# Kernel tuning notes

Measured on AMD Instinct MI355X. Metric: run time of the kernel, lower is better.

## Reference

```python
import jax, jax.numpy as jnp
import numpy as np

D_MODEL = 1024
N_HEADS = 16
D_HEAD = D_MODEL // N_HEADS
D_FF = 4096
B, T = 2, 2048


def layer_norm(x, gamma, beta, eps=1e-5):
    mu = jnp.mean(x, axis=-1, keepdims=True)
    var = jnp.var(x, axis=-1, keepdims=True)
    return (x - mu) * jax.lax.rsqrt(var + eps) * gamma + beta


def setup_inputs() -> dict:
    key = jax.random.key(0)
    ks = jax.random.split(key, 8)
    s = D_MODEL ** -0.5
    return {
        "x": jax.random.normal(ks[0], (B, T, D_MODEL), dtype=jnp.float32),
        "w_qkv": jax.random.normal(ks[1], (D_MODEL, 3 * D_MODEL), dtype=jnp.float32) * s,
        "w_out": jax.random.normal(ks[2], (D_MODEL, D_MODEL), dtype=jnp.float32) * s,
        "ln1_g": jnp.ones((D_MODEL,), jnp.float32),
        "ln1_b": jnp.zeros((D_MODEL,), jnp.float32),
        "ln2_g": jnp.ones((D_MODEL,), jnp.float32),
        "ln2_b": jnp.zeros((D_MODEL,), jnp.float32),
        "w1": jax.random.normal(ks[3], (D_MODEL, D_FF), dtype=jnp.float32) * s,
        "b1": jnp.zeros((D_FF,), jnp.float32),
        "w2": jax.random.normal(ks[4], (D_FF, D_MODEL), dtype=jnp.float32) * (D_FF ** -0.5),
        "b2": jnp.zeros((D_MODEL,), jnp.float32),
    }


def reference(x, w_qkv, w_out, ln1_g, ln1_b, ln2_g, ln2_b, w1, b1, w2, b2):
    Bb, Tt, C = x.shape
    h = layer_norm(x, ln1_g, ln1_b)
    qkv = h @ w_qkv  # [B,T,3C]
    q, k, v = jnp.split(qkv, 3, axis=-1)

    def heads(t):  # [B,T,C] -> [B,H,T,Dh]
        return t.reshape(Bb, Tt, N_HEADS, D_HEAD).transpose(0, 2, 1, 3)

    q, k, v = heads(q), heads(k), heads(v)
    scale = D_HEAD ** -0.5
    attn = jnp.einsum("bhqd,bhkd->bhqk", q, k) * scale
    causal = jnp.tril(jnp.ones((Tt, Tt), dtype=bool))
    attn = jnp.where(causal[None, None], attn, -jnp.inf)
    attn = jax.nn.softmax(attn, axis=-1)
    out = jnp.einsum("bhqk,bhkd->bhqd", attn, v)
    out = out.transpose(0, 2, 1, 3).reshape(Bb, Tt, C)
    x = x + out @ w_out
    h2 = layer_norm(x, ln2_g, ln2_b)
    ff = jax.nn.gelu(h2 @ w1 + b1, approximate=False) @ w2 + b2
    return x + ff
```

## Files before the change

kernel.cpp:

```cpp
#include <hip/hip_runtime.h>
#include <hip/hip_bf16.h>
#include <cstdint>

#define DM 1024
#define DFF 4096
#define NB 2
#define TT 2048
#define NH 16
#define DH 64

typedef unsigned short u16;
typedef __bf16 bf16x8 __attribute__((ext_vector_type(8)));
typedef float f32x4 __attribute__((ext_vector_type(4)));

__device__ __forceinline__ u16 f2b(float f) {
    union { float f; unsigned u; } v; v.f = f;
    unsigned u = v.u;
    return (u16)((u + 0x7FFFu + ((u >> 16) & 1u)) >> 16);
}

__device__ __forceinline__ float b2f(u16 u) {
    union { unsigned x; float f; } v;
    v.x = ((unsigned)u) << 16;
    return v.f;
}

__device__ __forceinline__ unsigned cvtpk(float a, float b) {
    unsigned r;
    asm("v_cvt_pk_bf16_f32 %0, %1, %2" : "=v"(r) : "v"(a), "v"(b));
    return r;
}

__device__ __forceinline__ float gelu_fast(float z) {
    const float u = z * z;
    const float w = z * __builtin_fmaf(u, 0.10294324f, 2.3022082f);
    const float e = exp2f(w);
    const float r = __builtin_amdgcn_rcpf(1.0f + e);
    return z - z * r;
}

__device__ __forceinline__ f32x4 mfma_bf16(bf16x8 a, bf16x8 b, f32x4 c) {
    return __builtin_amdgcn_mfma_f32_16x16x32_bf16(a, b, c, 0, 0, 0);
}

__device__ __forceinline__ void gload_lds16(const void* g, void* l) {
    __builtin_amdgcn_global_load_lds((const __attribute__((address_space(1))) unsigned int*)g,
                                     (__attribute__((address_space(3))) unsigned int*)l, 16, 0, 0);
}

__global__ __launch_bounds__(256) void prep_kernel(
    const float* __restrict__ wqkv, const float* __restrict__ wout,
    const float* __restrict__ w1, const float* __restrict__ w2,
    u16* __restrict__ wqkv_t, u16* __restrict__ wout_t,
    u16* __restrict__ w1_t, u16* __restrict__ w2_t,
    const float* __restrict__ x, const float* __restrict__ g,
    const float* __restrict__ bt, u16* __restrict__ H) {
    __shared__ float t[32][33];
    __shared__ float sb[8];
    const int id = blockIdx.x;
    const int tid = threadIdx.x;
    if (id < 12288) {
        const float* W;
        u16* Wt;
        int K, N, bx, by;
        if (id < 3072) {
            W = wqkv; Wt = wqkv_t; K = 1024; N = 3072; bx = id % 96; by = id / 96;
        } else if (id < 4096) {
            const int t2 = id - 3072;
            W = wout; Wt = wout_t; K = 1024; N = 1024; bx = t2 % 32; by = t2 / 32;
        } else if (id < 8192) {
            const int t2 = id - 4096;
            W = w1; Wt = w1_t; K = 1024; N = 4096; bx = t2 % 128; by = t2 / 128;
        } else {
            const int t2 = id - 8192;
            W = w2; Wt = w2_t; K = 4096; N = 1024; bx = t2 % 32; by = t2 / 32;
        }
        const int tx = tid & 31, ty = tid >> 5;
        const int k0 = by * 32, n0 = bx * 32;
#pragma unroll
        for (int j = 0; j < 4; ++j)
            t[ty + 8 * j][tx] = W[(size_t)(k0 + ty + 8 * j) * N + n0 + tx];
        __syncthreads();
#pragma unroll
        for (int j = 0; j < 4; ++j)
            Wt[(size_t)(n0 + ty + 8 * j) * K + k0 + tx] = f2b(t[tx][ty + 8 * j]);
    } else {
        const int row = id - 12288;
        float4 v = ((const float4*)(x + (size_t)row * DM))[tid];
        float s = v.x + v.y + v.z + v.w;
        float ss = v.x * v.x + v.y * v.y + v.z * v.z + v.w * v.w;
#pragma unroll
        for (int off = 32; off >= 1; off >>= 1) {
            s += __shfl_xor(s, off);
            ss += __shfl_xor(ss, off);
        }
        int w = tid >> 6, lane = tid & 63;
        if (lane == 0) { sb[w] = s; sb[4 + w] = ss; }
        __syncthreads();
        s = sb[0] + sb[1] + sb[2] + sb[3];
        ss = sb[4] + sb[5] + sb[6] + sb[7];
        float mu = s * (1.0f / DM);
        float var = ss * (1.0f / DM) - mu * mu;
        float rstd = rsqrtf(var + 1e-5f);
        float4 gv = ((const float4*)g)[tid];
        float4 bv = ((const float4*)bt)[tid];
        uint2 hv;
        hv.x = cvtpk((v.x - mu) * rstd * gv.x + bv.x, (v.y - mu) * rstd * gv.y + bv.y);
        hv.y = cvtpk((v.z - mu) * rstd * gv.z + bv.z, (v.w - mu) * rstd * gv.w + bv.w);
        ((uint2*)(H + (size_t)row * DM))[tid] = hv;
    }
}

__global__ __launch_bounds__(256) void ln_kernel(const float* __restrict__ X,
                                                 const float* __restrict__ g,
                                                 const float* __restrict__ bt,
                                                 u16* __restrict__ H) {
    int row = blockIdx.x, tid = threadIdx.x;
    float4 v = ((const float4*)(X + (size_t)row * DM))[tid];
    float s = v.x + v.y + v.z + v.w;
    float ss = v.x * v.x + v.y * v.y + v.z * v.z + v.w * v.w;
#pragma unroll
    for (int off = 32; off >= 1; off >>= 1) {
        s += __shfl_xor(s, off);
        ss += __shfl_xor(ss, off);
    }
    __shared__ float sb[8];
    int w = tid >> 6, lane = tid & 63;
    if (lane == 0) { sb[w] = s; sb[4 + w] = ss; }
    __syncthreads();
    s = sb[0] + sb[1] + sb[2] + sb[3];
    ss = sb[4] + sb[5] + sb[6] + sb[7];
    float mu = s * (1.0f / DM);
    float var = ss * (1.0f / DM) - mu * mu;
    float rstd = rsqrtf(var + 1e-5f);
    float4 gv = ((const float4*)g)[tid];
    float4 bv = ((const float4*)bt)[tid];
    uint2 hv;
    hv.x = cvtpk((v.x - mu) * rstd * gv.x + bv.x, (v.y - mu) * rstd * gv.y + bv.y);
    hv.y = cvtpk((v.z - mu) * rstd * gv.z + bv.z, (v.w - mu) * rstd * gv.w + bv.w);
    ((uint2*)(H + (size_t)row * DM))[tid] = hv;
}

__global__ __launch_bounds__(256) void add4_kernel(float* __restrict__ out,
                                                   const float* __restrict__ x1,
                                                   const float* __restrict__ b2,
                                                   const u16* __restrict__ p0,
                                                   const u16* __restrict__ p1,
                                                   const u16* __restrict__ p2,
                                                   const u16* __restrict__ p3, int n4) {
    int idx = blockIdx.x * 256 + threadIdx.x;
    const int stride = gridDim.x * 256;
    for (; idx < n4; idx += stride) {
        float4 a = ((const float4*)x1)[idx];
        const float4 bb = ((const float4*)b2)[idx & 255];
        ushort4 c0 = ((const ushort4*)p0)[idx];
        ushort4 c1 = ((const ushort4*)p1)[idx];
        ushort4 c2 = ((const ushort4*)p2)[idx];
        ushort4 c3 = ((const ushort4*)p3)[idx];
        a.x += bb.x + b2f(c0.x) + b2f(c1.x) + b2f(c2.x) + b2f(c3.x);
        a.y += bb.y + b2f(c0.y) + b2f(c1.y) + b2f(c2.y) + b2f(c3.y);
        a.z += bb.z + b2f(c0.z) + b2f(c1.z) + b2f(c2.z) + b2f(c3.z);
        a.w += bb.w + b2f(c0.w) + b2f(c1.w) + b2f(c2.w) + b2f(c3.w);
        ((float4*)out)[idx] = a;
    }
}

template <int MODE, int SPLIT>
__global__ __launch_bounds__(512, 2) void gemm256(
    const u16* __restrict__ A, const u16* __restrict__ Bt, int M, int N, int K,
    u16* __restrict__ oq, u16* __restrict__ ok, u16* __restrict__ vt,
    const float* __restrict__ bias, u16* __restrict__ outbf,
    u16* __restrict__ pb0, u16* __restrict__ pb1,
    u16* __restrict__ pb2, u16* __restrict__ pb3) {
    __shared__ __align__(16) u16 Alds[2][256][64];
    __shared__ __align__(16) u16 Blds[2][256][64];
    const int tid = threadIdx.x;
    const int lane = tid & 63, w = tid >> 6;
    const int wm = w >> 2, wn = w & 3;
    const int l15 = lane & 15, lg = lane >> 4;
    int bid = blockIdx.x + gridDim.x * blockIdx.y;
    const int nwg = gridDim.x * gridDim.y;
    bid = (bid & 7) * (nwg >> 3) + (bid >> 3);
    int mrow = bid / gridDim.x;
    int ks = 0;
    if constexpr (SPLIT > 1) {
        const int mtiles = (nwg / gridDim.x) / SPLIT;
        ks = mrow / mtiles;
        mrow -= ks * mtiles;
    }
    const int bm = mrow * 256, bn = (bid % gridDim.x) * 256;
    const int kbeg = SPLIT > 1 ? ks * (K / SPLIT) : 0;
    const int srow = tid >> 3, pch = tid & 7;
    const int lc = pch ^ (srow & 7);

    const u16* Ap = A + (size_t)(bm + srow) * K + kbeg + lc * 8;
    const u16* Bp = Bt + (size_t)(bn + srow) * K + kbeg + lc * 8;

    f32x4 acc[8][4] = {};
    bf16x8 bf[4][2];
    const int NT = (K / SPLIT) >> 6;

#define SA256(buf, t)                                                           \
    {                                                                           \
        _Pragma("unroll") for (int j = 0; j < 4; ++j)                           \
            gload_lds16(Ap + (size_t)(64 * j) * K + (t) * 64,                   \
                        &Alds[buf][srow + 64 * j][pch * 8]);                    \
    }
#define SB256(buf, t)                                                           \
    {                                                                           \
        _Pragma("unroll") for (int j = 0; j < 4; ++j)                           \
            gload_lds16(Bp + (size_t)(64 * j) * K + (t) * 64,                   \
                        &Blds[buf][srow + 64 * j][pch * 8]);                    \
    }

#define PHASE(BUF, P, STAGE, WAIT)                                              \
    {                                                                           \
        bf16x8 af[2][2];                                                        \
        _Pragma("unroll") for (int i = 0; i < 2; ++i) {                         \
            const int row = wm * 128 + (2 * (P) + i) * 16 + l15;                \
            _Pragma("unroll") for (int ks_ = 0; ks_ < 2; ++ks_)                 \
                af[i][ks_] =                                                    \
                    *(const bf16x8*)&Alds[BUF][row][((ks_ * 4 + lg) ^ (row & 7)) * 8]; \
        }                                                                       \
        if constexpr ((P) == 0) {                                               \
            _Pragma("unroll") for (int nf = 0; nf < 4; ++nf) {                  \
                const int row = wn * 64 + nf * 16 + l15;                        \
                _Pragma("unroll") for (int ks_ = 0; ks_ < 2; ++ks_)             \
                    bf[nf][ks_] =                                               \
                        *(const bf16x8*)&Blds[BUF][row][((ks_ * 4 + lg) ^ (row & 7)) * 8]; \
            }                                                                   \
        }                                                                       \
        STAGE;                                                                  \
        WAIT;                                                                   \
        __builtin_amdgcn_s_barrier();                                           \
        asm volatile("s_waitcnt lgkmcnt(0)" ::: "memory");                      \
        __builtin_amdgcn_sched_barrier(0);                                      \
        __builtin_amdgcn_s_setprio(1);                                          \
        _Pragma("unroll") for (int i = 0; i < 2; ++i)                           \
            _Pragma("unroll") for (int nf = 0; nf < 4; ++nf)                    \
                _Pragma("unroll") for (int ks_ = 0; ks_ < 2; ++ks_)             \
                    acc[2 * (P) + i][nf] =                                      \
                        mfma_bf16(af[i][ks_], bf[nf][ks_], acc[2 * (P) + i][nf]); \
        __builtin_amdgcn_s_setprio(0);                                          \
        __builtin_amdgcn_s_barrier();                                           \
    }

    SB256(0, 0);
    SA256(0, 0);
    SB256(1, 1);
    asm volatile("s_waitcnt vmcnt(4)" ::: "memory");
    __builtin_amdgcn_sched_barrier(0);
    __builtin_amdgcn_s_barrier();

    for (int it = 0; it < (NT >> 1); ++it) {
        const int t0 = 2 * it;
        const bool more = (t0 + 2 < NT);
        PHASE(0, 0, { SA256(1, t0 + 1); }, {});
        PHASE(0, 1, { if (more) SB256(0, t0 + 2); }, {});
        PHASE(0, 2, {}, {});
        PHASE(0, 3, {}, {
            if (more) { asm volatile("s_waitcnt vmcnt(4)" ::: "memory"); }
            else { asm volatile("s_waitcnt vmcnt(0)" ::: "memory"); }
            __builtin_amdgcn_sched_barrier(0);
        });
        PHASE(1, 0, { if (more) SA256(0, t0 + 2); }, {});
        PHASE(1, 1, { if (more) SB256(1, t0 + 3); }, {});
        PHASE(1, 2, {}, {});
        PHASE(1, 3, {}, {
            if (more) {
                asm volatile("s_waitcnt vmcnt(4)" ::: "memory");
                __builtin_amdgcn_sched_barrier(0);
            }
        });
    }
#undef PHASE
#undef SA256
#undef SB256

    const int m0 = bm + wm * 128, n0 = bn + wn * 64;
#pragma unroll
    for (int mi = 0; mi < 8; ++mi) {
#pragma unroll
        for (int ni = 0; ni < 4; ++ni) {
            if constexpr (MODE == 0) {
                const int n = n0 + ni * 16 + l15;
                const int which = n >> 10;
                const int hh = (n >> 6) & 15, d = n & 63;
                const int mbase = m0 + mi * 16 + 4 * lg;
                const int bb = mbase >> 11, t = mbase & 2047;
                if (which == 2) {
                    uint2 pv;
                    pv.x = cvtpk(acc[mi][ni][0], acc[mi][ni][1]);
                    pv.y = cvtpk(acc[mi][ni][2], acc[mi][ni][3]);
                    *(uint2*)(vt + (((size_t)(bb * NH + hh)) * DH + d) * TT + t) = pv;
                } else {
                    u16* dst = which == 0 ? oq : ok;
                    const float sc = which == 0 ? 0.18033688f : 1.0f;
                    const unsigned p01 = cvtpk(acc[mi][ni][0] * sc, acc[mi][ni][1] * sc);
                    const unsigned p23 = cvtpk(acc[mi][ni][2] * sc, acc[mi][ni][3] * sc);
                    u16* db = dst + (((size_t)(bb * NH + hh)) * TT + t) * DH + d;
                    db[0] = (u16)p01;
                    db[DH] = (u16)(p01 >> 16);
                    db[2 * DH] = (u16)p23;
                    db[3 * DH] = (u16)(p23 >> 16);
                }
            } else if constexpr (MODE == 2) {
                const int n = n0 + ni * 16 + l15;
                const float bn_ = bias[n];
                const float g0 = gelu_fast(acc[mi][ni][0] + bn_);
                const float g1 = gelu_fast(acc[mi][ni][1] + bn_);
                const float g2 = gelu_fast(acc[mi][ni][2] + bn_);
                const float g3 = gelu_fast(acc[mi][ni][3] + bn_);
                const unsigned p01 = cvtpk(g0, g1);
                const unsigned p23 = cvtpk(g2, g3);
                u16* db = outbf + (size_t)(m0 + mi * 16 + 4 * lg) * N + n;
                db[0] = (u16)p01;
                db[N] = (u16)(p01 >> 16);
                db[2 * N] = (u16)p23;
                db[3 * N] = (u16)(p23 >> 16);
            } else {
                const int n = n0 + ni * 16 + l15;
                u16* pb = ks == 0 ? pb0 : (ks == 1 ? pb1 : (ks == 2 ? pb2 : pb3));
                const unsigned q01 = cvtpk(acc[mi][ni][0], acc[mi][ni][1]);
                const unsigned q23 = cvtpk(acc[mi][ni][2], acc[mi][ni][3]);
                u16* db = pb + (size_t)(m0 + mi * 16 + 4 * lg) * N + n;
                db[0] = (u16)q01;
                db[N] = (u16)(q01 >> 16);
                db[2 * N] = (u16)q23;
                db[3 * N] = (u16)(q23 >> 16);
            }
        }
    }
}

template <int MODE>
__global__ __launch_bounds__(256) void gemm_kernel(
    const u16* __restrict__ A, const u16* __restrict__ Bt, int M, int N, int K,
    const float* __restrict__ resid, float* __restrict__ outf,
    const float* __restrict__ bias) {
    __shared__ __align__(16) u16 Alds[2][128][64];
    __shared__ __align__(16) u16 Blds[2][128][64];
    const int tid = threadIdx.x;
    const int lane = tid & 63;
    const int w = tid >> 6;
    const int wr = w >> 1, wc = w & 1;
    int bid = blockIdx.x + gridDim.x * blockIdx.y;
    const int nwg = gridDim.x * gridDim.y;
    bid = (bid & 7) * (nwg >> 3) + (bid >> 3);
    const int bm = (bid / gridDim.x) * 128, bn = (bid % gridDim.x) * 128;
    const int l15 = lane & 15, lg = lane >> 4;
    const int srow = tid >> 3, pch = tid & 7;
    const int lc = pch ^ (srow & 7);

    f32x4 acc[4][4] = {};
    const u16* Ap = A + (size_t)(bm + srow) * K + lc * 8;
    const u16* Bp = Bt + (size_t)(bn + srow) * K + lc * 8;

#define STAGE(buf, k0)                                                          \
    {                                                                           \
        _Pragma("unroll") for (int i = 0; i < 4; ++i) {                         \
            gload_lds16(Ap + (size_t)(32 * i) * K + (k0), &Alds[buf][srow + 32 * i][pch * 8]); \
            gload_lds16(Bp + (size_t)(32 * i) * K + (k0), &Blds[buf][srow + 32 * i][pch * 8]); \
        }                                                                       \
    }

#define COMPUTE(buf)                                                            \
    {                                                                           \
        _Pragma("unroll") for (int kk = 0; kk < 2; ++kk) {                      \
            bf16x8 af[4], bfr[4];                                               \
            _Pragma("unroll") for (int f = 0; f < 4; ++f) {                     \
                const int ar = wr * 64 + f * 16 + l15;                          \
                const int br = wc * 64 + f * 16 + l15;                          \
                const int kch = kk * 4 + lg;                                    \
                af[f] = *(const bf16x8*)&Alds[buf][ar][(kch ^ (ar & 7)) * 8];   \
                bfr[f] = *(const bf16x8*)&Blds[buf][br][(kch ^ (br & 7)) * 8];  \
            }                                                                   \
            _Pragma("unroll") for (int mi = 0; mi < 4; ++mi)                    \
                _Pragma("unroll") for (int ni = 0; ni < 4; ++ni)                \
                    acc[mi][ni] = mfma_bf16(af[mi], bfr[ni], acc[mi][ni]);      \
        }                                                                       \
    }

    STAGE(0, 0);
    for (int k0 = 0; k0 < K; k0 += 64) {
        const int cur = (k0 >> 6) & 1;
        if (k0 + 64 < K) {
            STAGE(cur ^ 1, k0 + 64);
            asm volatile("s_waitcnt vmcnt(8)" ::: "memory");
        } else {
            asm volatile("s_waitcnt vmcnt(0)" ::: "memory");
        }
        __builtin_amdgcn_sched_barrier(0);
        __builtin_amdgcn_s_barrier();
        __builtin_amdgcn_sched_barrier(0);
        COMPUTE(cur);
        __builtin_amdgcn_s_barrier();
    }
#undef STAGE
#undef COMPUTE

    const int m0 = bm + wr * 64, n0 = bn + wc * 64;
#pragma unroll
    for (int mi = 0; mi < 4; ++mi) {
#pragma unroll
        for (int ni = 0; ni < 4; ++ni) {
            const int n = n0 + ni * 16 + l15;
#pragma unroll
            for (int r = 0; r < 4; ++r) {
                const int m = m0 + mi * 16 + 4 * lg + r;
                const float v = acc[mi][ni][r];
                const size_t o = (size_t)m * N + n;
                if constexpr (MODE == 1) {
                    outf[o] = resid[o] + v;
                } else {
                    outf[o] = resid[o] + v + bias[n];
                }
            }
        }
    }
}

__global__ __launch_bounds__(256) void attn_kernel(const u16* __restrict__ Q,
                                                   const u16* __restrict__ Kg,
                                                   const u16* __restrict__ Vtg,
                                                   u16* __restrict__ O) {
    __shared__ __align__(16) u16 Klds[4][64][64];
    __shared__ __align__(16) u16 Vlds[4][64][64];
    const int tid = threadIdx.x, lane = tid & 63, w = tid >> 6;
    const int l15 = lane & 15, lg = lane >> 4;

    int id = blockIdx.x + (blockIdx.y << 4);
    int sw = (id & 7) * 64 + (id >> 3);
    const int p = sw & 15, bh = sw >> 4;
    const size_t base = (size_t)bh * TT * DH;
    const int b = bh >> 4, hh = bh & 15;

    const int srow = tid >> 3, pch = tid & 7;
    const int lc = pch ^ (srow & 7);

    const int vhalf = (lg & 1) * 8;
    const int vc = lg >> 1;

#define ASTAGE(buf, kv)                                                                     \
    {                                                                                       \
        gload_lds16(Kg + base + (size_t)((kv) * 64 + srow) * DH + lc * 8,                   \
                    &Klds[buf][srow][pch * 8]);                                             \
        gload_lds16(Kg + base + (size_t)((kv) * 64 + srow + 32) * DH + lc * 8,              \
                    &Klds[buf][srow + 32][pch * 8]);                                        \
        gload_lds16(Vtg + base + (size_t)srow * TT + (kv) * 64 + lc * 8,                    \
                    &Vlds[buf][srow][pch * 8]);                                             \
        gload_lds16(Vtg + base + (size_t)(srow + 32) * TT + (kv) * 64 + lc * 8,             \
                    &Vlds[buf][srow + 32][pch * 8]);                                        \
    }

    for (int half = 0; half < 2; ++half) {
        const int qt = half ? (31 - p) : p;
        const int nkv = qt + 1;
        const int qrow = qt * 64 + w * 16 + l15;
        uint4 qu0 = *(const uint4*)(Q + base + (size_t)qrow * DH + 8 * lg);
        uint4 qu1 = *(const uint4*)(Q + base + (size_t)qrow * DH + 32 + 8 * lg);
        asm volatile("" : "+v"(qu0.x), "+v"(qu0.y), "+v"(qu0.z), "+v"(qu0.w),
                          "+v"(qu1.x), "+v"(qu1.y), "+v"(qu1.z), "+v"(qu1.w));
        const bf16x8 qf0 = *(const bf16x8*)&qu0;
        const bf16x8 qf1 = *(const bf16x8*)&qu1;

        f32x4 o[4] = {};
        float lsum = 0.0f;

        auto compute_tile = [&](int buf, bool masked, int kvi) {
            f32x4 s[4] = {};
            __builtin_amdgcn_s_setprio(1);
#pragma unroll
            for (int nf = 0; nf < 4; ++nf) {
                const int row = nf * 16 + l15;
                bf16x8 kb0 = *(const bf16x8*)&Klds[buf][row][(lg ^ (l15 & 7)) * 8];
                bf16x8 kb1 = *(const bf16x8*)&Klds[buf][row][((4 + lg) ^ (l15 & 7)) * 8];
                s[nf] = mfma_bf16(kb0, qf0, s[nf]);
                s[nf] = mfma_bf16(kb1, qf1, s[nf]);
            }
            __builtin_amdgcn_s_setprio(0);

            if (masked) {
#pragma unroll
                for (int nf = 0; nf < 4; ++nf) {
                    const int tg = kvi * 64 + nf * 16 + 4 * lg;
#pragma unroll
                    for (int r = 0; r < 4; ++r)
                        if (tg + r > qrow) s[nf][r] = -1e30f;
                }
            }

            float ps = 0.0f;
#pragma unroll
            for (int nf = 0; nf < 4; ++nf) {
#pragma unroll
                for (int r = 0; r < 4; ++r) {
                    const float pp = exp2f(s[nf][r]);
                    s[nf][r] = pp;
                    ps += pp;
                }
            }
            lsum += ps;

            unsigned pk[4][2];
#pragma unroll
            for (int nf = 0; nf < 4; ++nf) {
                pk[nf][0] = cvtpk(s[nf][0], s[nf][1]);
                pk[nf][1] = cvtpk(s[nf][2], s[nf][3]);
            }
            uint4 pu0, pu1;
            pu0.x = pk[0][0]; pu0.y = pk[0][1]; pu0.z = pk[1][0]; pu0.w = pk[1][1];
            pu1.x = pk[2][0]; pu1.y = pk[2][1]; pu1.z = pk[3][0]; pu1.w = pk[3][1];
            const bf16x8 pa0 = *(const bf16x8*)&pu0;
            const bf16x8 pa1 = *(const bf16x8*)&pu1;

            __builtin_amdgcn_s_setprio(1);
#pragma unroll
            for (int nf = 0; nf < 4; ++nf) {
                const int row = nf * 16 + l15;
                const int swz = row & 7;
                const char* vb = (const char*)&Vlds[buf][row][0];
                uint2 a0 = *(const uint2*)(vb + (((vc + 0) ^ swz) * 16 + vhalf));
                uint2 a1 = *(const uint2*)(vb + (((vc + 2) ^ swz) * 16 + vhalf));
                uint2 b0 = *(const uint2*)(vb + (((vc + 4) ^ swz) * 16 + vhalf));
                uint2 b1 = *(const uint2*)(vb + (((vc + 6) ^ swz) * 16 + vhalf));
                uint4 v0; v0.x = a0.x; v0.y = a0.y; v0.z = a1.x; v0.w = a1.y;
                uint4 v1; v1.x = b0.x; v1.y = b0.y; v1.z = b1.x; v1.w = b1.y;
                o[nf] = mfma_bf16(*(const bf16x8*)&v0, pa0, o[nf]);
                o[nf] = mfma_bf16(*(const bf16x8*)&v1, pa1, o[nf]);
            }
            __builtin_amdgcn_s_setprio(0);
        };

        ASTAGE(0, 0);
        if (nkv > 1) ASTAGE(1, 1);

        for (int kv = 0; kv < nkv; kv += 2) {
            int nst = 0;
            if (kv + 2 < nkv) { ASTAGE((kv + 2) & 3, kv + 2); nst += 4; }
            if (kv + 3 < nkv) { ASTAGE((kv + 3) & 3, kv + 3); nst += 4; }
            if (nst == 8)
                asm volatile("s_waitcnt vmcnt(8)" ::: "memory");
            else if (nst == 4)
                asm volatile("s_waitcnt vmcnt(4)" ::: "memory");
            else
                asm volatile("s_waitcnt vmcnt(0)" ::: "memory");
            __builtin_amdgcn_sched_barrier(0);
            __builtin_amdgcn_s_barrier();
            __builtin_amdgcn_sched_barrier(0);

            compute_tile(kv & 3, kv == qt, kv);
            if (kv + 1 < nkv) compute_tile((kv + 1) & 3, kv + 1 == qt, kv + 1);

            __builtin_amdgcn_s_barrier();
        }

        lsum += __shfl_xor(lsum, 16);
        lsum += __shfl_xor(lsum, 32);
        const float linv = 1.0f / lsum;
#pragma unroll
        for (int nf = 0; nf < 4; ++nf) {
            uint2 pv;
            pv.x = cvtpk(o[nf][0] * linv, o[nf][1] * linv);
            pv.y = cvtpk(o[nf][2] * linv, o[nf][3] * linv);
            *(uint2*)(O + ((size_t)b * TT + qrow) * DM + hh * DH + nf * 16 + 4 * lg) = pv;
        }
    }
#undef ASTAGE
}

extern "C" void kernel_launch(void* const* d_in, const int* in_sizes, int n_in,
                              void* d_out, int out_size, void* d_ws, size_t ws_size,
                              hipStream_t stream) {
    const float* x = (const float*)d_in[0];
    const float* wqkv = (const float*)d_in[1];
    const float* wout = (const float*)d_in[2];
    const float* ln1g = (const float*)d_in[3];
    const float* ln1b = (const float*)d_in[4];
    const float* ln2g = (const float*)d_in[5];
    const float* ln2b = (const float*)d_in[6];
    const float* w1 = (const float*)d_in[7];
    const float* b1 = (const float*)d_in[8];
    const float* w2 = (const float*)d_in[9];
    const float* b2 = (const float*)d_in[10];
    float* out = (float*)d_out;
    char* ws = (char*)d_ws;

    u16* wqkv_t = (u16*)(ws + 0);
    u16* wout_t = (u16*)(ws + 6291456);
    u16* w1_t   = (u16*)(ws + 8388608);
    u16* w2_t   = (u16*)(ws + 16777216);
    u16* h_bf   = (u16*)(ws + 25165824);
    u16* q_bf   = (u16*)(ws + 33554432);
    u16* k_bf   = (u16*)(ws + 41943040);
    u16* vt_bf  = (u16*)(ws + 50331648);
    u16* at_bf  = (u16*)(ws + 58720256);
    float* x1   = (float*)(ws + 67108864);
    u16* ff1_bf = q_bf;
    u16* pb0 = (u16*)(ws + 58720256);
    u16* pb1 = (u16*)(ws + 0);
    u16* pb2 = (u16*)(ws + 8388608);
    u16* pb3 = (u16*)(ws + 25165824);

    prep_kernel<<<16384, 256, 0, stream>>>(wqkv, wout, w1, w2,
                                           wqkv_t, wout_t, w1_t, w2_t,
                                           x, ln1g, ln1b, h_bf);

    gemm256<0, 1><<<dim3(12, 16), 512, 0, stream>>>(h_bf, wqkv_t, 4096, 3072, 1024,
                                                    q_bf, k_bf, vt_bf, nullptr, nullptr,
                                                    nullptr, nullptr, nullptr, nullptr);

    attn_kernel<<<dim3(16, 32), 256, 0, stream>>>(q_bf, k_bf, vt_bf, at_bf);

    gemm_kernel<1><<<dim3(8, 32), 256, 0, stream>>>(at_bf, wout_t, 4096, 1024, 1024,
                                                    x, x1, nullptr);

    ln_kernel<<<4096, 256, 0, stream>>>(x1, ln2g, ln2b, h_bf);

    gemm256<2, 1><<<dim3(16, 16), 512, 0, stream>>>(h_bf, w1_t, 4096, 4096, 1024,
                                                    nullptr, nullptr, nullptr, b1, ff1_bf,
                                                    nullptr, nullptr, nullptr, nullptr);

    gemm256<3, 4><<<dim3(4, 64), 512, 0, stream>>>(ff1_bf, w2_t, 4096, 1024, 4096,
                                                   nullptr, nullptr, nullptr, nullptr, nullptr,
                                                   pb0, pb1, pb2, pb3);

    add4_kernel<<<2048, 256, 0, stream>>>(out, x1, b2, pb0, pb1, pb2, pb3,
                                          4096 * 1024 / 4);
}
```

Baseline: 221.7 us.

## Split attention to one query tile per block with double-buffered KV

Each attention block previously handled a pair of query tiles (p and 31-p) to balance causal work. Now each block handles one query tile, the grid doubles to 1024 blocks, and the KV pipeline drops from 4 to 2 LDS buffers with one tile processed per iteration. The intent is more parallelism and lower LDS use, which allows more resident blocks per CU. In exchange, work per block is uneven, so load balance depends on the hardware scheduler, and the prefetch depth is shallower.

```diff
diff --git a/kernel.cpp b/kernel.cpp
--- a/kernel.cpp
+++ b/kernel.cpp
@@ -424,14 +424,15 @@
                                                    const u16* __restrict__ Kg,
                                                    const u16* __restrict__ Vtg,
                                                    u16* __restrict__ O) {
-    __shared__ __align__(16) u16 Klds[4][64][64];
-    __shared__ __align__(16) u16 Vlds[4][64][64];
+    __shared__ __align__(16) u16 Klds[2][64][64];
+    __shared__ __align__(16) u16 Vlds[2][64][64];
     const int tid = threadIdx.x, lane = tid & 63, w = tid >> 6;
     const int l15 = lane & 15, lg = lane >> 4;
 
-    int id = blockIdx.x + (blockIdx.y << 4);
-    int sw = (id & 7) * 64 + (id >> 3);
-    const int p = sw & 15, bh = sw >> 4;
+    int id = blockIdx.x + (blockIdx.y << 5);
+    int sw = (id & 7) * 128 + (id >> 3);
+    const int qt = sw & 31, bh = sw >> 5;
+    const int nkv = qt + 1;
     const size_t base = (size_t)bh * TT * DH;
     const int b = bh >> 4, hh = bh & 15;
 
@@ -453,118 +454,107 @@
                     &Vlds[buf][srow + 32][pch * 8]);                                        \
     }
 
-    for (int half = 0; half < 2; ++half) {
-        const int qt = half ? (31 - p) : p;
-        const int nkv = qt + 1;
-        const int qrow = qt * 64 + w * 16 + l15;
-        uint4 qu0 = *(const uint4*)(Q + base + (size_t)qrow * DH + 8 * lg);
-        uint4 qu1 = *(const uint4*)(Q + base + (size_t)qrow * DH + 32 + 8 * lg);
-        asm volatile("" : "+v"(qu0.x), "+v"(qu0.y), "+v"(qu0.z), "+v"(qu0.w),
-                          "+v"(qu1.x), "+v"(qu1.y), "+v"(qu1.z), "+v"(qu1.w));
-        const bf16x8 qf0 = *(const bf16x8*)&qu0;
-        const bf16x8 qf1 = *(const bf16x8*)&qu1;
-
-        f32x4 o[4] = {};
-        float lsum = 0.0f;
-
-        auto compute_tile = [&](int buf, bool masked, int kvi) {
-            f32x4 s[4] = {};
-            __builtin_amdgcn_s_setprio(1);
+    const int qrow = qt * 64 + w * 16 + l15;
+    uint4 qu0 = *(const uint4*)(Q + base + (size_t)qrow * DH + 8 * lg);
+    uint4 qu1 = *(const uint4*)(Q + base + (size_t)qrow * DH + 32 + 8 * lg);
+    asm volatile("" : "+v"(qu0.x), "+v"(qu0.y), "+v"(qu0.z), "+v"(qu0.w),
+                      "+v"(qu1.x), "+v"(qu1.y), "+v"(qu1.z), "+v"(qu1.w));
+    const bf16x8 qf0 = *(const bf16x8*)&qu0;
+    const bf16x8 qf1 = *(const bf16x8*)&qu1;
+
+    f32x4 o[4] = {};
+    float lsum = 0.0f;
+
+    ASTAGE(0, 0);
+
+    int cur = 0;
+    for (int kv = 0; kv < nkv; ++kv) {
+        if (kv + 1 < nkv) {
+            ASTAGE(cur ^ 1, kv + 1);
+            asm volatile("s_waitcnt vmcnt(4)" ::: "memory");
+        } else {
+            asm volatile("s_waitcnt vmcnt(0)" ::: "memory");
+        }
+        __builtin_amdgcn_sched_barrier(0);
+        __builtin_amdgcn_s_barrier();
+        __builtin_amdgcn_sched_barrier(0);
+
+        f32x4 s[4] = {};
+        __builtin_amdgcn_s_setprio(1);
+#pragma unroll
+        for (int nf = 0; nf < 4; ++nf) {
+            const int row = nf * 16 + l15;
+            bf16x8 kb0 = *(const bf16x8*)&Klds[cur][row][(lg ^ (l15 & 7)) * 8];
+            bf16x8 kb1 = *(const bf16x8*)&Klds[cur][row][((4 + lg) ^ (l15 & 7)) * 8];
+            s[nf] = mfma_bf16(kb0, qf0, s[nf]);
+            s[nf] = mfma_bf16(kb1, qf1, s[nf]);
+        }
+        __builtin_amdgcn_s_setprio(0);
+
+        if (kv == qt) {
 #pragma unroll
             for (int nf = 0; nf < 4; ++nf) {
-                const int row = nf * 16 + l15;
-                bf16x8 kb0 = *(const bf16x8*)&Klds[buf][row][(lg ^ (l15 & 7)) * 8];
-                bf16x8 kb1 = *(const bf16x8*)&Klds[buf][row][((4 + lg) ^ (l15 & 7)) * 8];
-                s[nf] = mfma_bf16(kb0, qf0, s[nf]);
-                s[nf] = mfma_bf16(kb1, qf1, s[nf]);
+                const int tg = kv * 64 + nf * 16 + 4 * lg;
+#pragma unroll
+                for (int r = 0; r < 4; ++r)
+                    if (tg + r > qrow) s[nf][r] = -1e30f;
             }
-            __builtin_amdgcn_s_setprio(0);
-
-            if (masked) {
-#pragma unroll
-                for (int nf = 0; nf < 4; ++nf) {
-                    const int tg = kvi * 64 + nf * 16 + 4 * lg;
-#pragma unroll
-                    for (int r = 0; r < 4; ++r)
-                        if (tg + r > qrow) s[nf][r] = -1e30f;
-                }
+        }
+
+        float ps = 0.0f;
+#pragma unroll
+        for (int nf = 0; nf < 4; ++nf) {
+#pragma unroll
+            for (int r = 0; r < 4; ++r) {
+                const float pp = exp2f(s[nf][r]);
+                s[nf][r] = pp;
+                ps += pp;
             }
-
-            float ps = 0.0f;
-#pragma unroll
-            for (int nf = 0; nf < 4; ++nf) {
-#pragma unroll
-                for (int r = 0; r < 4; ++r) {
-                    const float pp = exp2f(s[nf][r]);
-                    s[nf][r] = pp;
-                    ps += pp;
-                }
-            }
-            lsum += ps;
-
-            unsigned pk[4][2];
-#pragma unroll
-            for (int nf = 0; nf < 4; ++nf) {
-                pk[nf][0] = cvtpk(s[nf][0], s[nf][1]);
-                pk[nf][1] = cvtpk(s[nf][2], s[nf][3]);
-            }
-            uint4 pu0, pu1;
-            pu0.x = pk[0][0]; pu0.y = pk[0][1]; pu0.z = pk[1][0]; pu0.w = pk[1][1];
-            pu1.x = pk[2][0]; pu1.y = pk[2][1]; pu1.z = pk[3][0]; pu1.w = pk[3][1];
-            const bf16x8 pa0 = *(const bf16x8*)&pu0;
-            const bf16x8 pa1 = *(const bf16x8*)&pu1;
-
-            __builtin_amdgcn_s_setprio(1);
-#pragma unroll
-            for (int nf = 0; nf < 4; ++nf) {
-                const int row = nf * 16 + l15;
-                const int swz = row & 7;
-                const char* vb = (const char*)&Vlds[buf][row][0];
-                uint2 a0 = *(const uint2*)(vb + (((vc + 0) ^ swz) * 16 + vhalf));
-                uint2 a1 = *(const uint2*)(vb + (((vc + 2) ^ swz) * 16 + vhalf));
-                uint2 b0 = *(const uint2*)(vb + (((vc + 4) ^ swz) * 16 + vhalf));
-                uint2 b1 = *(const uint2*)(vb + (((vc + 6) ^ swz) * 16 + vhalf));
-                uint4 v0; v0.x = a0.x; v0.y = a0.y; v0.z = a1.x; v0.w = a1.y;
-                uint4 v1; v1.x = b0.x; v1.y = b0.y; v1.z = b1.x; v1.w = b1.y;
-                o[nf] = mfma_bf16(*(const bf16x8*)&v0, pa0, o[nf]);
-                o[nf] = mfma_bf16(*(const bf16x8*)&v1, pa1, o[nf]);
-            }
-            __builtin_amdgcn_s_setprio(0);
-        };
-
-        ASTAGE(0, 0);
-        if (nkv > 1) ASTAGE(1, 1);
-
-        for (int kv = 0; kv < nkv; kv += 2) {
-            int nst = 0;
-            if (kv + 2 < nkv) { ASTAGE((kv + 2) & 3, kv + 2); nst += 4; }
-            if (kv + 3 < nkv) { ASTAGE((kv + 3) & 3, kv + 3); nst += 4; }
-            if (nst == 8)
-                asm volatile("s_waitcnt vmcnt(8)" ::: "memory");
-            else if (nst == 4)
-                asm volatile("s_waitcnt vmcnt(4)" ::: "memory");
-            else
-                asm volatile("s_waitcnt vmcnt(0)" ::: "memory");
-            __builtin_amdgcn_sched_barrier(0);
-            __builtin_amdgcn_s_barrier();
-            __builtin_amdgcn_sched_barrier(0);
-
-            compute_tile(kv & 3, kv == qt, kv);
-            if (kv + 1 < nkv) compute_tile((kv + 1) & 3, kv + 1 == qt, kv + 1);
-
-            __builtin_amdgcn_s_barrier();
-        }
-
-        lsum += __shfl_xor(lsum, 16);
-        lsum += __shfl_xor(lsum, 32);
-        const float linv = 1.0f / lsum;
+        }
+        lsum += ps;
+
+        unsigned pk[4][2];
 #pragma unroll
         for (int nf = 0; nf < 4; ++nf) {
-            uint2 pv;
-            pv.x = cvtpk(o[nf][0] * linv, o[nf][1] * linv);
-            pv.y = cvtpk(o[nf][2] * linv, o[nf][3] * linv);
-            *(uint2*)(O + ((size_t)b * TT + qrow) * DM + hh * DH + nf * 16 + 4 * lg) = pv;
-        }
+            pk[nf][0] = cvtpk(s[nf][0], s[nf][1]);
+            pk[nf][1] = cvtpk(s[nf][2], s[nf][3]);
+        }
+        uint4 pu0, pu1;
+        pu0.x = pk[0][0]; pu0.y = pk[0][1]; pu0.z = pk[1][0]; pu0.w = pk[1][1];
+        pu1.x = pk[2][0]; pu1.y = pk[2][1]; pu1.z = pk[3][0]; pu1.w = pk[3][1];
+        const bf16x8 pa0 = *(const bf16x8*)&pu0;
+        const bf16x8 pa1 = *(const bf16x8*)&pu1;
+
+        __builtin_amdgcn_s_setprio(1);
+#pragma unroll
+        for (int nf = 0; nf < 4; ++nf) {
+            const int row = nf * 16 + l15;
+            const int swz = row & 7;
+            const char* vb = (const char*)&Vlds[cur][row][0];
+            uint2 a0 = *(const uint2*)(vb + (((vc + 0) ^ swz) * 16 + vhalf));
+            uint2 a1 = *(const uint2*)(vb + (((vc + 2) ^ swz) * 16 + vhalf));
+            uint2 b0 = *(const uint2*)(vb + (((vc + 4) ^ swz) * 16 + vhalf));
+            uint2 b1 = *(const uint2*)(vb + (((vc + 6) ^ swz) * 16 + vhalf));
+            uint4 v0; v0.x = a0.x; v0.y = a0.y; v0.z = a1.x; v0.w = a1.y;
+            uint4 v1; v1.x = b0.x; v1.y = b0.y; v1.z = b1.x; v1.w = b1.y;
+            o[nf] = mfma_bf16(*(const bf16x8*)&v0, pa0, o[nf]);
+            o[nf] = mfma_bf16(*(const bf16x8*)&v1, pa1, o[nf]);
+        }
+        __builtin_amdgcn_s_setprio(0);
+
+        __builtin_amdgcn_s_barrier();
+        cur ^= 1;
+    }
+
+    lsum += __shfl_xor(lsum, 16);
+    lsum += __shfl_xor(lsum, 32);
+    const float linv = 1.0f / lsum;
+#pragma unroll
+    for (int nf = 0; nf < 4; ++nf) {
+        uint2 pv;
+        pv.x = cvtpk(o[nf][0] * linv, o[nf][1] * linv);
+        pv.y = cvtpk(o[nf][2] * linv, o[nf][3] * linv);
+        *(uint2*)(O + ((size_t)b * TT + qrow) * DM + hh * DH + nf * 16 + 4 * lg) = pv;
     }
 #undef ASTAGE
 }
@@ -610,7 +600,7 @@
                                                     q_bf, k_bf, vt_bf, nullptr, nullptr,
                                                     nullptr, nullptr, nullptr, nullptr);
 
-    attn_kernel<<<dim3(16, 32), 256, 0, stream>>>(q_bf, k_bf, vt_bf, at_bf);
+    attn_kernel<<<dim3(32, 32), 256, 0, stream>>>(q_bf, k_bf, vt_bf, at_bf);
 
     gemm_kernel<1><<<dim3(8, 32), 256, 0, stream>>>(at_bf, wout_t, 4096, 1024, 1024,
                                                     x, x1, nullptr);
```

Result: slower. 247.4 us (+11.6%).
